# Kernel tuning notes

Measured on AMD Instinct MI355X. Metric: run time of the kernel, lower is better.

The kernel has to match this reference:

```python
import jax, jax.numpy as jnp
import numpy as np

N, E, B = 50000, 1600000, 64
VOCAB, EMB = 1000, 16
HID, OUT_FEAT = 192, 128   # hidden_sf*model_dim, out_sf*output_channels
MODEL_DIM, DEMO, OUT_DIM = 64, 5, 2
EPS = 1e-7  # GENConv eps


def setup_inputs() -> dict:
    key = jax.random.key(0)
    ks = jax.random.split(key, 18)
    f32 = jnp.float32

    def rn(k, shape, scale):
        return jax.random.normal(k, shape, dtype=f32) * scale

    node_idx = jax.random.randint(ks[0], (N,), 0, VOCAB)
    edge_index = jax.random.randint(ks[1], (2, E), 0, N)
    batch = jnp.sort(jax.random.randint(ks[2], (N,), 0, B))
    demographics = rn(ks[3], (B, DEMO), 1.0)

    emb = rn(ks[4], (VOCAB, EMB), 1.0)
    dims = [(EMB, HID), (HID, HID), (HID, HID), (HID, OUT_FEAT)]
    params = {}
    for i, (din, dout) in enumerate(dims):
        params[f"W{i}"] = rn(ks[5 + 2 * i], (din, dout), 1.0 / np.sqrt(din))
        params[f"b{i}"] = jnp.zeros((dout,), f32)
    params["Wc1"] = rn(ks[13], (OUT_FEAT + DEMO, MODEL_DIM), 1.0 / np.sqrt(OUT_FEAT + DEMO))
    params["bc1"] = jnp.zeros((MODEL_DIM,), f32)
    params["Wc2"] = rn(ks[14], (MODEL_DIM, OUT_DIM), 1.0 / np.sqrt(MODEL_DIM))
    params["bc2"] = jnp.zeros((OUT_DIM,), f32)

    return {"node_idx": node_idx, "edge_index": edge_index, "batch": batch,
            "demographics": demographics, "emb": emb, **params}


def _gen_conv(x, src, dst, W, b):
    # GENConv (num_layers=1, aggr='add', edge_attr=None):
    #   out_i = Linear( sum_{j->i} (relu(x_j) + eps) + x_i )
    m = jax.nn.relu(x) + EPS                                   # [N, D]
    agg = jax.ops.segment_sum(m[src], dst, num_segments=x.shape[0])
    return (agg + x) @ W + b


def reference(node_idx, edge_index, batch, demographics, emb,
              W0, b0, W1, b1, W2, b2, W3, b3, Wc1, bc1, Wc2, bc2):
    x = emb[node_idx]                                          # [N, 16]
    src, dst = edge_index[0], edge_index[1]
    for W, b in ((W0, b0), (W1, b1), (W2, b2), (W3, b3)):
        x = _gen_conv(x, src, dst, W, b)                       # [N, D_l]
    # global_mean_pool
    cnt = jax.ops.segment_sum(jnp.ones((x.shape[0],), x.dtype), batch, num_segments=B)
    g = jax.ops.segment_sum(x, batch, num_segments=B) / jnp.maximum(cnt, 1.0)[:, None]
    feats = jnp.concatenate([g, demographics], axis=1)         # [B, 133]
    h = jax.nn.relu(feats @ Wc1 + bc1)                         # dropout = identity (eval)
    return h @ Wc2 + bc2                                       # [B, out_dim]
```

## Files before the change

kernel.cpp:

```cpp
#include <hip/hip_runtime.h>
#include <stdint.h>

#define EPS 1e-7f

constexpr int N_NODES = 50000;
constexpr int N_EDGES = 1600000;
constexpr int BATCH = 64;
constexpr int EMB = 16;
constexpr int HID = 192;
constexpr int OUTF = 128;
constexpr int DEMO = 5;
constexpr int MODEL_DIM = 64;
constexpr int OUT_DIM = 2;

constexpr int NPART = 8;
constexpr int PART_NODES = (N_NODES + NPART - 1) / NPART;

constexpr int NBKT = 16;
constexpr int BKT_DIV = (N_NODES + NBKT - 1) / NBKT;
constexpr int NB2 = N_NODES * NBKT;

constexpr int SCAN2_CHUNK = 1024;
constexpr int NCHUNK2 = (NB2 + SCAN2_CHUNK - 1) / SCAN2_CHUNK;

typedef unsigned short bf16_t;
typedef short s8v __attribute__((ext_vector_type(8)));
typedef float f4v __attribute__((ext_vector_type(4)));

static __device__ __forceinline__ float bf2f(bf16_t u) {
  return __uint_as_float(((uint32_t)u) << 16);
}
static __device__ __forceinline__ bf16_t f2bf(float f) {
  uint32_t b = __float_as_uint(f);
  return (bf16_t)((b + 0x7FFFu + ((b >> 16) & 1u)) >> 16);
}

__global__ void emb_gather(const int* __restrict__ idx, const float* __restrict__ emb,
                           bf16_t* __restrict__ x) {
  int t = blockIdx.x * blockDim.x + threadIdx.x;
  if (t >= N_NODES * EMB) return;
  int node = t / EMB, f = t % EMB;
  x[t] = f2bf(emb[idx[node] * EMB + f]);
}

__global__ void hist2_kernel(const int* __restrict__ src, const int* __restrict__ dst,
                             int* __restrict__ hist2) {
  int part = blockIdx.x & (NPART - 1);
  int blk = blockIdx.x >> 3;
  int nthread = (gridDim.x >> 3) * blockDim.x;
  int lo = part * PART_NODES, hi = lo + PART_NODES;
  for (int e = blk * blockDim.x + threadIdx.x; e < N_EDGES; e += nthread) {
    int d = dst[e];
    if (d >= lo && d < hi) atomicAdd(&hist2[d * NBKT + src[e] / BKT_DIV], 1);
  }
}

__global__ void chunk_sum2_kernel(const int* __restrict__ hist2, int* __restrict__ chunk_sum) {
  int t = threadIdx.x;
  int base = blockIdx.x * SCAN2_CHUNK + t * 4;
  int v = 0;
#pragma unroll
  for (int j = 0; j < 4; ++j) {
    int i = base + j;
    if (i < NB2) v += hist2[i];
  }
#pragma unroll
  for (int off = 32; off > 0; off >>= 1) v += __shfl_down(v, off);
  __shared__ int s[4];
  if ((t & 63) == 0) s[t >> 6] = v;
  __syncthreads();
  if (t == 0) chunk_sum[blockIdx.x] = s[0] + s[1] + s[2] + s[3];
}

__global__ void scan_chunks2_kernel(const int* __restrict__ chunk_sum,
                                    int* __restrict__ chunk_off) {
  __shared__ int s[1024];
  int t = threadIdx.x;
  int v = (t < NCHUNK2) ? chunk_sum[t] : 0;
  s[t] = v;
  __syncthreads();
  for (int off = 1; off < 1024; off <<= 1) {
    int u = (t >= off) ? s[t - off] : 0;
    __syncthreads();
    s[t] += u;
    __syncthreads();
  }
  if (t < NCHUNK2) chunk_off[t] = s[t] - v;
}

__global__ void chunk_scan_write2_kernel(const int* __restrict__ hist2,
                                         const int* __restrict__ chunk_off,
                                         int* __restrict__ cursor2,
                                         int* __restrict__ row_start) {
  __shared__ int s[256];
  int t = threadIdx.x;
  int base = blockIdx.x * SCAN2_CHUNK + t * 4;
  int local[4];
  int tsum = 0;
#pragma unroll
  for (int j = 0; j < 4; ++j) {
    int i = base + j;
    local[j] = (i < NB2) ? hist2[i] : 0;
    tsum += local[j];
  }
  s[t] = tsum;
  __syncthreads();
  for (int off = 1; off < 256; off <<= 1) {
    int u = (t >= off) ? s[t - off] : 0;
    __syncthreads();
    s[t] += u;
    __syncthreads();
  }
  int run = chunk_off[blockIdx.x] + s[t] - tsum;
#pragma unroll
  for (int j = 0; j < 4; ++j) {
    int i = base + j;
    if (i < NB2) {
      cursor2[i] = run;
      if ((i & (NBKT - 1)) == 0) row_start[i / NBKT] = run;
      if (i == NB2 - 1) row_start[N_NODES] = run + local[j];
      run += local[j];
    }
  }
}

__global__ void scatter_kernel(const int* __restrict__ src, const int* __restrict__ dst,
                               int* __restrict__ cursor2, int* __restrict__ csr_src) {
  int part = blockIdx.x & (NPART - 1);
  int blk = blockIdx.x >> 3;
  int nthread = (gridDim.x >> 3) * blockDim.x;
  int lo = part * PART_NODES, hi = lo + PART_NODES;
  for (int e = blk * blockDim.x + threadIdx.x; e < N_EDGES; e += nthread) {
    int d = dst[e];
    if (d >= lo && d < hi) {
      int s = src[e];
      int pos = atomicAdd(&cursor2[d * NBKT + s / BKT_DIV], 1);
      csr_src[pos] = s;
    }
  }
}

template <int TPN, int NPB>
__global__ void agg2_kernel(const uint32_t* __restrict__ x, const int* __restrict__ row_start,
                            const int* __restrict__ csr_src, uint32_t* __restrict__ out) {
  int f = threadIdx.x % TPN;
  int node = blockIdx.x * NPB + threadIdx.x / TPN;
  if (node >= N_NODES) return;
  int s0 = row_start[node], s1 = row_start[node + 1];
  float deps = (float)(s1 - s0) * EPS;
  uint32_t xv = x[(size_t)node * TPN + f];
  float a0 = __uint_as_float(xv << 16) + deps;
  float a1 = __uint_as_float(xv & 0xFFFF0000u) + deps;
  int e = s0;
  for (; e + 8 <= s1; e += 8) {
    int idx[8];
#pragma unroll
    for (int j = 0; j < 8; ++j) idx[j] = csr_src[e + j];
    uint32_t v[8];
#pragma unroll
    for (int j = 0; j < 8; ++j) v[j] = x[(size_t)idx[j] * TPN + f];
#pragma unroll
    for (int j = 0; j < 8; ++j) {
      a0 += fmaxf(__uint_as_float(v[j] << 16), 0.f);
      a1 += fmaxf(__uint_as_float(v[j] & 0xFFFF0000u), 0.f);
    }
  }
  for (; e < s1; ++e) {
    uint32_t v = x[(size_t)csr_src[e] * TPN + f];
    a0 += fmaxf(__uint_as_float(v << 16), 0.f);
    a1 += fmaxf(__uint_as_float(v & 0xFFFF0000u), 0.f);
  }
  out[(size_t)node * TPN + f] = (uint32_t)f2bf(a0) | ((uint32_t)f2bf(a1) << 16);
}

constexpr int A4_TPN = 24;
constexpr int A4_NPB = 8;
__global__ void agg4_kernel(const uint4* __restrict__ x, const int* __restrict__ row_start,
                            const int* __restrict__ csr_src, uint4* __restrict__ out) {
  constexpr int ROW = 24;
  int f = threadIdx.x % A4_TPN;
  int node = blockIdx.x * A4_NPB + threadIdx.x / A4_TPN;
  if (node >= N_NODES) return;
  int s0 = row_start[node], s1 = row_start[node + 1];
  float deps = (float)(s1 - s0) * EPS;
  uint4 xv = x[(size_t)node * ROW + f];
  float a[8];
  {
    uint32_t pk[4] = {xv.x, xv.y, xv.z, xv.w};
#pragma unroll
    for (int q = 0; q < 4; ++q) {
      a[2 * q]     = __uint_as_float(pk[q] << 16) + deps;
      a[2 * q + 1] = __uint_as_float(pk[q] & 0xFFFF0000u) + deps;
    }
  }
  int e = s0;
  for (; e + 4 <= s1; e += 4) {
    int idx[4];
#pragma unroll
    for (int j = 0; j < 4; ++j) idx[j] = csr_src[e + j];
    uint4 v[4];
#pragma unroll
    for (int j = 0; j < 4; ++j) v[j] = x[(size_t)idx[j] * ROW + f];
#pragma unroll
    for (int j = 0; j < 4; ++j) {
      uint32_t pk[4] = {v[j].x, v[j].y, v[j].z, v[j].w};
#pragma unroll
      for (int q = 0; q < 4; ++q) {
        a[2 * q]     += fmaxf(__uint_as_float(pk[q] << 16), 0.f);
        a[2 * q + 1] += fmaxf(__uint_as_float(pk[q] & 0xFFFF0000u), 0.f);
      }
    }
  }
  for (; e < s1; ++e) {
    uint4 v = x[(size_t)csr_src[e] * ROW + f];
    uint32_t pk[4] = {v.x, v.y, v.z, v.w};
#pragma unroll
    for (int q = 0; q < 4; ++q) {
      a[2 * q]     += fmaxf(__uint_as_float(pk[q] << 16), 0.f);
      a[2 * q + 1] += fmaxf(__uint_as_float(pk[q] & 0xFFFF0000u), 0.f);
    }
  }
  uint4 o;
  o.x = (uint32_t)f2bf(a[0]) | ((uint32_t)f2bf(a[1]) << 16);
  o.y = (uint32_t)f2bf(a[2]) | ((uint32_t)f2bf(a[3]) << 16);
  o.z = (uint32_t)f2bf(a[4]) | ((uint32_t)f2bf(a[5]) << 16);
  o.w = (uint32_t)f2bf(a[6]) | ((uint32_t)f2bf(a[7]) << 16);
  out[(size_t)node * ROW + f] = o;
}

__global__ void wprep_kernel(const float* __restrict__ W, int K, int NOUT,
                             bf16_t* __restrict__ Wt) {
  int t = blockIdx.x * blockDim.x + threadIdx.x;
  if (t >= K * NOUT) return;
  int k = t / NOUT, n = t % NOUT;
  Wt[(size_t)n * K + k] = f2bf(W[t]);
}

template <int NOUT, bool OUT_BF16>
__global__ void mfma_gemm(const bf16_t* __restrict__ in, const bf16_t* __restrict__ Wt,
                          const float* __restrict__ bias, void* __restrict__ outp) {
  constexpr int K = 192;
  constexpr int KT = K / 32;
  constexpr int NT = NOUT / 16;
  int wave = threadIdx.x >> 6;
  int lane = threadIdx.x & 63;
  int tile = blockIdx.x * 4 + wave;
  if (tile >= N_NODES / 16) return;

  int rlo = lane & 15;
  int kbase = (lane >> 4) * 8;

  s8v a[KT];
  const bf16_t* ap = in + ((size_t)(tile * 16 + rlo)) * K + kbase;
#pragma unroll
  for (int kt = 0; kt < KT; ++kt) a[kt] = *(const s8v*)(ap + kt * 32);

  int r0 = (lane >> 4) * 4;
#pragma unroll
  for (int nt = 0; nt < NT; ++nt) {
    const bf16_t* wp = Wt + ((size_t)(nt * 16 + rlo)) * K + kbase;
    f4v c = {0.f, 0.f, 0.f, 0.f};
#pragma unroll
    for (int kt = 0; kt < KT; ++kt) {
      s8v b = *(const s8v*)(wp + kt * 32);
      c = __builtin_amdgcn_mfma_f32_16x16x32_bf16(a[kt], b, c, 0, 0, 0);
    }
    float bv = bias[nt * 16 + rlo];
#pragma unroll
    for (int r = 0; r < 4; ++r) {
      float v = c[r] + bv;
      size_t o = (size_t)(tile * 16 + r0 + r) * NOUT + nt * 16 + rlo;
      if constexpr (OUT_BF16) ((bf16_t*)outp)[o] = f2bf(v);
      else                    ((float*)outp)[o] = v;
    }
  }
}

template <int DIN, int DOUT, bool OUT_BF16>
__global__ void gemm_kernel(const bf16_t* __restrict__ in, const float* __restrict__ W,
                            const float* __restrict__ bias, void* __restrict__ outp) {
  constexpr int ROWS = 16;
  __shared__ bf16_t tile[ROWS * DIN];
  int c = threadIdx.x;
  int base = blockIdx.x * ROWS;

  {
    const uint4* gsrc = reinterpret_cast<const uint4*>(in + (size_t)base * DIN);
    uint4* ldst = reinterpret_cast<uint4*>(tile);
    constexpr int NV = ROWS * DIN * 2 / 16;
    for (int i = threadIdx.x; i < NV; i += blockDim.x) ldst[i] = gsrc[i];
  }
  __syncthreads();

  float acc[ROWS];
  float bc = bias[c];
#pragma unroll
  for (int r = 0; r < ROWS; ++r) acc[r] = bc;

  for (int k0 = 0; k0 < DIN; k0 += 8) {
    float w[8];
#pragma unroll
    for (int j = 0; j < 8; ++j) w[j] = W[(size_t)(k0 + j) * DOUT + c];
#pragma unroll
    for (int r = 0; r < ROWS; ++r) {
      uint4 packed = *reinterpret_cast<const uint4*>(&tile[r * DIN + k0]);
      uint32_t pk[4] = {packed.x, packed.y, packed.z, packed.w};
#pragma unroll
      for (int q = 0; q < 4; ++q) {
        float lo = __uint_as_float(pk[q] << 16);
        float hi = __uint_as_float(pk[q] & 0xFFFF0000u);
        acc[r] = fmaf(lo, w[2 * q], acc[r]);
        acc[r] = fmaf(hi, w[2 * q + 1], acc[r]);
      }
    }
  }

#pragma unroll
  for (int r = 0; r < ROWS; ++r) {
    size_t o = (size_t)(base + r) * DOUT + c;
    if constexpr (OUT_BF16) ((bf16_t*)outp)[o] = f2bf(acc[r]);
    else                    ((float*)outp)[o] = acc[r];
  }
}

constexpr int POOL_CHUNK = 100;
__global__ void pool_kernel(const float* __restrict__ x, const int* __restrict__ batch,
                            float* __restrict__ gsum, int* __restrict__ gcnt) {
  int f = threadIdx.x;
  int start = blockIdx.x * POOL_CHUNK;
  if (start >= N_NODES) return;
  int end = min(start + POOL_CHUNK, N_NODES);
  int cur = batch[start];
  float acc = 0.f;
  int cnt = 0;
  for (int i = start; i < end; ++i) {
    int b = batch[i];
    if (b != cur) {
      atomicAdd(&gsum[cur * OUTF + f], acc);
      if (f == 0) atomicAdd(&gcnt[cur], cnt);
      acc = 0.f; cnt = 0; cur = b;
    }
    acc += x[(size_t)i * OUTF + f];
    cnt++;
  }
  atomicAdd(&gsum[cur * OUTF + f], acc);
  if (f == 0) atomicAdd(&gcnt[cur], cnt);
}

__global__ void mlp_kernel(const float* __restrict__ gsum, const int* __restrict__ gcnt,
                           const float* __restrict__ demo,
                           const float* __restrict__ Wc1, const float* __restrict__ bc1,
                           const float* __restrict__ Wc2, const float* __restrict__ bc2,
                           float* __restrict__ out) {
  int b = blockIdx.x;
  int c = threadIdx.x;
  __shared__ float feats[OUTF + DEMO];
  float inv = 1.f / fmaxf((float)gcnt[b], 1.f);
  for (int k = c; k < OUTF; k += MODEL_DIM) feats[k] = gsum[b * OUTF + k] * inv;
  if (c < DEMO) feats[OUTF + c] = demo[b * DEMO + c];
  __syncthreads();
  float s = bc1[c];
#pragma unroll
  for (int k = 0; k < OUTF + DEMO; ++k) s = fmaf(feats[k], Wc1[k * MODEL_DIM + c], s);
  float h = fmaxf(s, 0.f);
  float o0 = h * Wc2[c * OUT_DIM + 0];
  float o1 = h * Wc2[c * OUT_DIM + 1];
#pragma unroll
  for (int off = 32; off > 0; off >>= 1) {
    o0 += __shfl_down(o0, off);
    o1 += __shfl_down(o1, off);
  }
  if (c == 0) {
    out[b * OUT_DIM + 0] = o0 + bc2[0];
    out[b * OUT_DIM + 1] = o1 + bc2[1];
  }
}

extern "C" void kernel_launch(void* const* d_in, const int* in_sizes, int n_in,
                              void* d_out, int out_size, void* d_ws, size_t ws_size,
                              hipStream_t stream) {
  const int*   node_idx = (const int*)d_in[0];
  const int*   edge_index = (const int*)d_in[1];
  const int*   batch = (const int*)d_in[2];
  const float* demo = (const float*)d_in[3];
  const float* emb  = (const float*)d_in[4];
  const float* W0 = (const float*)d_in[5];  const float* b0 = (const float*)d_in[6];
  const float* W1 = (const float*)d_in[7];  const float* b1 = (const float*)d_in[8];
  const float* W2 = (const float*)d_in[9];  const float* b2 = (const float*)d_in[10];
  const float* W3 = (const float*)d_in[11]; const float* b3 = (const float*)d_in[12];
  const float* Wc1 = (const float*)d_in[13]; const float* bc1 = (const float*)d_in[14];
  const float* Wc2 = (const float*)d_in[15]; const float* bc2 = (const float*)d_in[16];
  const int* src = edge_index;
  const int* dst = edge_index + N_EDGES;
  float* out = (float*)d_out;

  char* ws = (char*)d_ws;
  size_t off = 0;
  auto alloc = [&](size_t bytes) {
    void* p = ws + off;
    off += (bytes + 255) & ~size_t(255);
    return p;
  };
  bf16_t* xbf     = (bf16_t*)alloc((size_t)N_NODES * HID * 2);
  bf16_t* aggbf   = (bf16_t*)alloc((size_t)N_NODES * HID * 2);
  float*  x3      = (float*)alloc((size_t)N_NODES * OUTF * 4);
  int*   csr_src  = (int*)alloc((size_t)N_EDGES * 4);
  int*   hist2    = (int*)alloc((size_t)NB2 * 4);
  int*   cursor2  = (int*)alloc((size_t)NB2 * 4);
  int*   row_start= (int*)alloc((size_t)(N_NODES + 1) * 4);
  int*   chunk_sum= (int*)alloc((size_t)NCHUNK2 * 4);
  int*   chunk_off= (int*)alloc((size_t)NCHUNK2 * 4);
  float* gsum     = (float*)alloc((size_t)BATCH * OUTF * 4);
  int*   gcnt     = (int*)alloc((size_t)BATCH * 4);
  bf16_t* Wt1     = (bf16_t*)alloc((size_t)HID * HID * 2);
  bf16_t* Wt2     = (bf16_t*)alloc((size_t)HID * HID * 2);
  bf16_t* Wt3     = (bf16_t*)alloc((size_t)OUTF * HID * 2);

  hipMemsetAsync(hist2, 0, (size_t)NB2 * 4, stream);
  hipMemsetAsync(gsum, 0, (size_t)BATCH * OUTF * 4, stream);
  hipMemsetAsync(gcnt, 0, (size_t)BATCH * 4, stream);

  wprep_kernel<<<(HID * HID + 255) / 256, 256, 0, stream>>>(W1, HID, HID, Wt1);
  wprep_kernel<<<(HID * HID + 255) / 256, 256, 0, stream>>>(W2, HID, HID, Wt2);
  wprep_kernel<<<(HID * OUTF + 255) / 256, 256, 0, stream>>>(W3, HID, OUTF, Wt3);

  hist2_kernel<<<NPART * 256, 256, 0, stream>>>(src, dst, hist2);
  chunk_sum2_kernel<<<NCHUNK2, 256, 0, stream>>>(hist2, chunk_sum);
  scan_chunks2_kernel<<<1, 1024, 0, stream>>>(chunk_sum, chunk_off);
  chunk_scan_write2_kernel<<<NCHUNK2, 256, 0, stream>>>(hist2, chunk_off, cursor2, row_start);
  scatter_kernel<<<NPART * 256, 256, 0, stream>>>(src, dst, cursor2, csr_src);

  constexpr int TILES = N_NODES / 16;
  constexpr int GBLK = (TILES + 3) / 4;
  constexpr int A4_GRID = (N_NODES + A4_NPB - 1) / A4_NPB;

  emb_gather<<<(N_NODES * EMB + 255) / 256, 256, 0, stream>>>(node_idx, emb, xbf);
  agg2_kernel<8, 32><<<(N_NODES + 31) / 32, 256, 0, stream>>>(
      (const uint32_t*)xbf, row_start, csr_src, (uint32_t*)aggbf);
  gemm_kernel<16, 192, true><<<N_NODES / 16, 192, 0, stream>>>(aggbf, W0, b0, xbf);
  agg4_kernel<<<A4_GRID, A4_TPN * A4_NPB, 0, stream>>>(
      (const uint4*)xbf, row_start, csr_src, (uint4*)aggbf);
  mfma_gemm<192, true><<<GBLK, 256, 0, stream>>>(aggbf, Wt1, b1, xbf);
  agg4_kernel<<<A4_GRID, A4_TPN * A4_NPB, 0, stream>>>(
      (const uint4*)xbf, row_start, csr_src, (uint4*)aggbf);
  mfma_gemm<192, true><<<GBLK, 256, 0, stream>>>(aggbf, Wt2, b2, xbf);
  agg4_kernel<<<A4_GRID, A4_TPN * A4_NPB, 0, stream>>>(
      (const uint4*)xbf, row_start, csr_src, (uint4*)aggbf);
  mfma_gemm<128, false><<<GBLK, 256, 0, stream>>>(aggbf, Wt3, b3, x3);

  pool_kernel<<<(N_NODES + POOL_CHUNK - 1) / POOL_CHUNK, OUTF, 0, stream>>>(x3, batch, gsum, gcnt);
  mlp_kernel<<<BATCH, MODEL_DIM, 0, stream>>>(gsum, gcnt, demo, Wc1, bc1, Wc2, bc2, out);
}
```

Measured before the change: 557.9 us.

## Fuse neighbor aggregation with MFMA GEMM for hidden GENConv layers

Merges the agg4 aggregation kernel and the MFMA linear layer into a single kernel per hidden layer. Each block of 384 threads aggregates 16 nodes into a padded LDS tile, then six waves split the output column tiles with MFMA. This removes the round trip of the aggregated features through global memory and halves the launch count. Because input and output can no longer share a buffer, features now ping-pong between two buffers. The cost is larger blocks with LDS use, and every block re-reads the weight matrix.

```diff
diff --git a/kernel.cpp b/kernel.cpp
--- a/kernel.cpp
+++ b/kernel.cpp
@@ -173,61 +173,6 @@
   out[(size_t)node * TPN + f] = (uint32_t)f2bf(a0) | ((uint32_t)f2bf(a1) << 16);
 }
 
-constexpr int A4_TPN = 24;
-constexpr int A4_NPB = 8;
-__global__ void agg4_kernel(const uint4* __restrict__ x, const int* __restrict__ row_start,
-                            const int* __restrict__ csr_src, uint4* __restrict__ out) {
-  constexpr int ROW = 24;
-  int f = threadIdx.x % A4_TPN;
-  int node = blockIdx.x * A4_NPB + threadIdx.x / A4_TPN;
-  if (node >= N_NODES) return;
-  int s0 = row_start[node], s1 = row_start[node + 1];
-  float deps = (float)(s1 - s0) * EPS;
-  uint4 xv = x[(size_t)node * ROW + f];
-  float a[8];
-  {
-    uint32_t pk[4] = {xv.x, xv.y, xv.z, xv.w};
-#pragma unroll
-    for (int q = 0; q < 4; ++q) {
-      a[2 * q]     = __uint_as_float(pk[q] << 16) + deps;
-      a[2 * q + 1] = __uint_as_float(pk[q] & 0xFFFF0000u) + deps;
-    }
-  }
-  int e = s0;
-  for (; e + 4 <= s1; e += 4) {
-    int idx[4];
-#pragma unroll
-    for (int j = 0; j < 4; ++j) idx[j] = csr_src[e + j];
-    uint4 v[4];
-#pragma unroll
-    for (int j = 0; j < 4; ++j) v[j] = x[(size_t)idx[j] * ROW + f];
-#pragma unroll
-    for (int j = 0; j < 4; ++j) {
-      uint32_t pk[4] = {v[j].x, v[j].y, v[j].z, v[j].w};
-#pragma unroll
-      for (int q = 0; q < 4; ++q) {
-        a[2 * q]     += fmaxf(__uint_as_float(pk[q] << 16), 0.f);
-        a[2 * q + 1] += fmaxf(__uint_as_float(pk[q] & 0xFFFF0000u), 0.f);
-      }
-    }
-  }
-  for (; e < s1; ++e) {
-    uint4 v = x[(size_t)csr_src[e] * ROW + f];
-    uint32_t pk[4] = {v.x, v.y, v.z, v.w};
-#pragma unroll
-    for (int q = 0; q < 4; ++q) {
-      a[2 * q]     += fmaxf(__uint_as_float(pk[q] << 16), 0.f);
-      a[2 * q + 1] += fmaxf(__uint_as_float(pk[q] & 0xFFFF0000u), 0.f);
-    }
-  }
-  uint4 o;
-  o.x = (uint32_t)f2bf(a[0]) | ((uint32_t)f2bf(a[1]) << 16);
-  o.y = (uint32_t)f2bf(a[2]) | ((uint32_t)f2bf(a[3]) << 16);
-  o.z = (uint32_t)f2bf(a[4]) | ((uint32_t)f2bf(a[5]) << 16);
-  o.w = (uint32_t)f2bf(a[6]) | ((uint32_t)f2bf(a[7]) << 16);
-  out[(size_t)node * ROW + f] = o;
-}
-
 __global__ void wprep_kernel(const float* __restrict__ W, int K, int NOUT,
                              bf16_t* __restrict__ Wt) {
   int t = blockIdx.x * blockDim.x + threadIdx.x;
@@ -236,42 +181,101 @@
   Wt[(size_t)n * K + k] = f2bf(W[t]);
 }
 
+constexpr int FU_TPN = 24;
+constexpr int FU_NPB = 16;
+constexpr int FU_LDR = 200;
 template <int NOUT, bool OUT_BF16>
-__global__ void mfma_gemm(const bf16_t* __restrict__ in, const bf16_t* __restrict__ Wt,
-                          const float* __restrict__ bias, void* __restrict__ outp) {
+__global__ void fused_agg_gemm(const uint4* __restrict__ x, const int* __restrict__ row_start,
+                               const int* __restrict__ csr_src,
+                               const bf16_t* __restrict__ Wt, const float* __restrict__ bias,
+                               void* __restrict__ outp) {
   constexpr int K = 192;
-  constexpr int KT = K / 32;
-  constexpr int NT = NOUT / 16;
-  int wave = threadIdx.x >> 6;
-  int lane = threadIdx.x & 63;
-  int tile = blockIdx.x * 4 + wave;
-  if (tile >= N_NODES / 16) return;
-
-  int rlo = lane & 15;
-  int kbase = (lane >> 4) * 8;
-
-  s8v a[KT];
-  const bf16_t* ap = in + ((size_t)(tile * 16 + rlo)) * K + kbase;
-#pragma unroll
-  for (int kt = 0; kt < KT; ++kt) a[kt] = *(const s8v*)(ap + kt * 32);
-
-  int r0 = (lane >> 4) * 4;
-#pragma unroll
-  for (int nt = 0; nt < NT; ++nt) {
-    const bf16_t* wp = Wt + ((size_t)(nt * 16 + rlo)) * K + kbase;
-    f4v c = {0.f, 0.f, 0.f, 0.f};
-#pragma unroll
-    for (int kt = 0; kt < KT; ++kt) {
-      s8v b = *(const s8v*)(wp + kt * 32);
-      c = __builtin_amdgcn_mfma_f32_16x16x32_bf16(a[kt], b, c, 0, 0, 0);
-    }
-    float bv = bias[nt * 16 + rlo];
-#pragma unroll
-    for (int r = 0; r < 4; ++r) {
-      float v = c[r] + bv;
-      size_t o = (size_t)(tile * 16 + r0 + r) * NOUT + nt * 16 + rlo;
-      if constexpr (OUT_BF16) ((bf16_t*)outp)[o] = f2bf(v);
-      else                    ((float*)outp)[o] = v;
+  constexpr int ROW = 24;
+  __shared__ bf16_t tile[FU_NPB * FU_LDR];
+
+  {
+    int f = threadIdx.x % FU_TPN;
+    int ln = threadIdx.x / FU_TPN;
+    int node = blockIdx.x * FU_NPB + ln;
+    int s0 = row_start[node], s1 = row_start[node + 1];
+    float deps = (float)(s1 - s0) * EPS;
+    uint4 xv = x[(size_t)node * ROW + f];
+    float a[8];
+    {
+      uint32_t pk[4] = {xv.x, xv.y, xv.z, xv.w};
+#pragma unroll
+      for (int q = 0; q < 4; ++q) {
+        a[2 * q]     = __uint_as_float(pk[q] << 16) + deps;
+        a[2 * q + 1] = __uint_as_float(pk[q] & 0xFFFF0000u) + deps;
+      }
+    }
+    int e = s0;
+    for (; e + 4 <= s1; e += 4) {
+      int idx[4];
+#pragma unroll
+      for (int j = 0; j < 4; ++j) idx[j] = csr_src[e + j];
+      uint4 v[4];
+#pragma unroll
+      for (int j = 0; j < 4; ++j) v[j] = x[(size_t)idx[j] * ROW + f];
+#pragma unroll
+      for (int j = 0; j < 4; ++j) {
+        uint32_t pk[4] = {v[j].x, v[j].y, v[j].z, v[j].w};
+#pragma unroll
+        for (int q = 0; q < 4; ++q) {
+          a[2 * q]     += fmaxf(__uint_as_float(pk[q] << 16), 0.f);
+          a[2 * q + 1] += fmaxf(__uint_as_float(pk[q] & 0xFFFF0000u), 0.f);
+        }
+      }
+    }
+    for (; e < s1; ++e) {
+      uint4 v = x[(size_t)csr_src[e] * ROW + f];
+      uint32_t pk[4] = {v.x, v.y, v.z, v.w};
+#pragma unroll
+      for (int q = 0; q < 4; ++q) {
+        a[2 * q]     += fmaxf(__uint_as_float(pk[q] << 16), 0.f);
+        a[2 * q + 1] += fmaxf(__uint_as_float(pk[q] & 0xFFFF0000u), 0.f);
+      }
+    }
+    uint4 o;
+    o.x = (uint32_t)f2bf(a[0]) | ((uint32_t)f2bf(a[1]) << 16);
+    o.y = (uint32_t)f2bf(a[2]) | ((uint32_t)f2bf(a[3]) << 16);
+    o.z = (uint32_t)f2bf(a[4]) | ((uint32_t)f2bf(a[5]) << 16);
+    o.w = (uint32_t)f2bf(a[6]) | ((uint32_t)f2bf(a[7]) << 16);
+    *reinterpret_cast<uint4*>(&tile[ln * FU_LDR + f * 8]) = o;
+  }
+  __syncthreads();
+
+  {
+    constexpr int KT = K / 32;
+    constexpr int NT = NOUT / 16;
+    int wave = threadIdx.x >> 6;
+    int lane = threadIdx.x & 63;
+    int rlo = lane & 15;
+    int kbase = (lane >> 4) * 8;
+
+    s8v af[KT];
+#pragma unroll
+    for (int kt = 0; kt < KT; ++kt)
+      af[kt] = *reinterpret_cast<const s8v*>(&tile[rlo * FU_LDR + kbase + kt * 32]);
+
+    int r0 = (lane >> 4) * 4;
+    for (int nt = wave; nt < NT; nt += 6) {
+      const bf16_t* wp = Wt + ((size_t)(nt * 16 + rlo)) * K + kbase;
+      f4v c = {0.f, 0.f, 0.f, 0.f};
+#pragma unroll
+      for (int kt = 0; kt < KT; ++kt) {
+        s8v b = *(const s8v*)(wp + kt * 32);
+        c = __builtin_amdgcn_mfma_f32_16x16x32_bf16(af[kt], b, c, 0, 0, 0);
+      }
+      int col = nt * 16 + rlo;
+      float bv = bias[col];
+#pragma unroll
+      for (int r = 0; r < 4; ++r) {
+        float v = c[r] + bv;
+        size_t o = (size_t)(blockIdx.x * FU_NPB + r0 + r) * NOUT + col;
+        if constexpr (OUT_BF16) ((bf16_t*)outp)[o] = f2bf(v);
+        else                    ((float*)outp)[o] = v;
+      }
     }
   }
 }
@@ -402,7 +406,9 @@
     return p;
   };
   bf16_t* xbf     = (bf16_t*)alloc((size_t)N_NODES * HID * 2);
-  bf16_t* aggbf   = (bf16_t*)alloc((size_t)N_NODES * HID * 2);
+  bf16_t* xbf2    = (bf16_t*)alloc((size_t)N_NODES * HID * 2);
+  bf16_t* xbf0    = (bf16_t*)alloc((size_t)N_NODES * EMB * 2);
+  bf16_t* agg0    = (bf16_t*)alloc((size_t)N_NODES * EMB * 2);
   float*  x3      = (float*)alloc((size_t)N_NODES * OUTF * 4);
   int*   csr_src  = (int*)alloc((size_t)N_EDGES * 4);
   int*   hist2    = (int*)alloc((size_t)NB2 * 4);
@@ -430,23 +436,18 @@
   chunk_scan_write2_kernel<<<NCHUNK2, 256, 0, stream>>>(hist2, chunk_off, cursor2, row_start);
   scatter_kernel<<<NPART * 256, 256, 0, stream>>>(src, dst, cursor2, csr_src);
 
-  constexpr int TILES = N_NODES / 16;
-  constexpr int GBLK = (TILES + 3) / 4;
-  constexpr int A4_GRID = (N_NODES + A4_NPB - 1) / A4_NPB;
-
-  emb_gather<<<(N_NODES * EMB + 255) / 256, 256, 0, stream>>>(node_idx, emb, xbf);
+  constexpr int FU_GRID = N_NODES / FU_NPB;
+
+  emb_gather<<<(N_NODES * EMB + 255) / 256, 256, 0, stream>>>(node_idx, emb, xbf0);
   agg2_kernel<8, 32><<<(N_NODES + 31) / 32, 256, 0, stream>>>(
-      (const uint32_t*)xbf, row_start, csr_src, (uint32_t*)aggbf);
-  gemm_kernel<16, 192, true><<<N_NODES / 16, 192, 0, stream>>>(aggbf, W0, b0, xbf);
-  agg4_kernel<<<A4_GRID, A4_TPN * A4_NPB, 0, stream>>>(
-      (const uint4*)xbf, row_start, csr_src, (uint4*)aggbf);
-  mfma_gemm<192, true><<<GBLK, 256, 0, stream>>>(aggbf, Wt1, b1, xbf);
-  agg4_kernel<<<A4_GRID, A4_TPN * A4_NPB, 0, stream>>>(
-      (const uint4*)xbf, row_start, csr_src, (uint4*)aggbf);
-  mfma_gemm<192, true><<<GBLK, 256, 0, stream>>>(aggbf, Wt2, b2, xbf);
-  agg4_kernel<<<A4_GRID, A4_TPN * A4_NPB, 0, stream>>>(
-      (const uint4*)xbf, row_start, csr_src, (uint4*)aggbf);
-  mfma_gemm<128, false><<<GBLK, 256, 0, stream>>>(aggbf, Wt3, b3, x3);
+      (const uint32_t*)xbf0, row_start, csr_src, (uint32_t*)agg0);
+  gemm_kernel<16, 192, true><<<N_NODES / 16, 192, 0, stream>>>(agg0, W0, b0, xbf);
+  fused_agg_gemm<192, true><<<FU_GRID, FU_TPN * FU_NPB, 0, stream>>>(
+      (const uint4*)xbf, row_start, csr_src, Wt1, b1, xbf2);
+  fused_agg_gemm<192, true><<<FU_GRID, FU_TPN * FU_NPB, 0, stream>>>(
+      (const uint4*)xbf2, row_start, csr_src, Wt2, b2, xbf);
+  fused_agg_gemm<128, false><<<FU_GRID, FU_TPN * FU_NPB, 0, stream>>>(
+      (const uint4*)xbf, row_start, csr_src, Wt3, b3, x3);
 
   pool_kernel<<<(N_NODES + POOL_CHUNK - 1) / POOL_CHUNK, OUTF, 0, stream>>>(x3, batch, gsum, gcnt);
   mlp_kernel<<<BATCH, MODEL_DIM, 0, stream>>>(gsum, gcnt, demo, Wc1, bc1, Wc2, bc2, out);
```

Result: faster. 501.6 us (-10.1%).
